# Kernel tuning notes

Hardware: AMD Instinct MI355X
Metric: run time of the kernel (lower is better)

## Reference

```python
import jax, jax.numpy as jnp
import numpy as np

BN_EPS = 1e-5

def _sign(x):
    # torch-style binarize with sign(0) -> +1 (deterministic)
    return jnp.where(x >= 0, 1.0, -1.0).astype(x.dtype)

def _binarize(x):
    # straight-through estimator: forward = sign(x), backward = identity
    return x + jax.lax.stop_gradient(_sign(x) - x)

def setup_inputs() -> dict:
    key = jax.random.key(0)
    k1, k2, k3, k4 = jax.random.split(key, 4)
    B, Cin, H, Wd = 64, 512, 32, 32  # Cin = in_planes*2
    Cout = 256                        # planes == in_planes
    x = jax.random.normal(k1, (B, Cin, H, Wd), jnp.float32)
    W = jax.random.normal(k2, (Cout, Cin, 3, 3), jnp.float32) * 0.05
    gamma = 1.0 + 0.1 * jax.random.normal(k3, (Cout,), jnp.float32)
    beta = 0.1 * jax.random.normal(k4, (Cout,), jnp.float32)
    return {"x": x, "W": W, "gamma": gamma, "beta": beta}

def reference(x, W, gamma, beta):
    inplanes = x.shape[1] // 2
    residual = x[:, :inplanes]  # first half of channels, pre-binarization
    xb = _binarize(x)
    wb = _binarize(W)
    out = jax.lax.conv_general_dilated(
        xb, wb, window_strides=(1, 1), padding=((1, 1), (1, 1)),
        dimension_numbers=("NCHW", "OIHW", "NCHW"))
    # BatchNorm2d in training mode (batch statistics over N,H,W per channel)
    mean = out.mean(axis=(0, 2, 3), keepdims=True)
    var = out.var(axis=(0, 2, 3), keepdims=True)
    out = (out - mean) * jax.lax.rsqrt(var + BN_EPS)
    out = out * gamma[None, :, None, None] + beta[None, :, None, None]
    out = out + residual
    return jnp.clip(out, -1.0, 1.0)  # Hardtanh
```

## Files before the change

kernel.cpp:

```cpp
#include <hip/hip_runtime.h>

#define CIN   512
#define COUT  256
#define HWDIM 32
#define NBATCH 64
#define PIX_PER_IMG (HWDIM * HWDIM)
#define NPIX (NBATCH * PIX_PER_IMG)

typedef __attribute__((ext_vector_type(4))) int   i32x4;
typedef __attribute__((ext_vector_type(8))) int   i32x8;
typedef __attribute__((ext_vector_type(4))) float f32x4;

#define OFF_XB4   ((size_t)0)
#define OFF_WB4   ((size_t)16777216)
#define OFF_CONV  ((size_t)17367040)
#define OFF_STATS ((size_t)50921472)
#define OFF_SCALE (OFF_STATS + 24576)
#define OFF_SHIFT (OFF_SCALE + 1024)
#define OFF_ZERO  (OFF_SHIFT + 1024)

#define NIB(v) ((v) >= 0.f ? 0x2u : 0xAu)

__global__ __launch_bounds__(256) void pack_x4_kernel(const float* __restrict__ x,
                                                      unsigned char* __restrict__ xb4) {
  const int plane = blockIdx.x;
  const int n = plane >> 5, h = plane & 31;
  __shared__ unsigned int tile[HWDIM * 66];
  const int t = threadIdx.x;
  const float* xp = x + (size_t)n * CIN * PIX_PER_IMG + (size_t)h * HWDIM;
#pragma unroll
  for (int it = 0; it < 2; ++it) {
    int idx = it * 256 + t;
    int cib = idx >> 3;
    int w4 = (idx & 7) << 2;
    unsigned n0 = 0, n1 = 0, n2 = 0, n3 = 0;
#pragma unroll
    for (int d = 0; d < 8; ++d) {
      float4 f = *reinterpret_cast<const float4*>(
          xp + (size_t)(cib * 8 + d) * PIX_PER_IMG + w4);
      n0 |= NIB(f.x) << (4 * d);
      n1 |= NIB(f.y) << (4 * d);
      n2 |= NIB(f.z) << (4 * d);
      n3 |= NIB(f.w) << (4 * d);
    }
    tile[(w4 + 0) * 66 + cib] = n0;
    tile[(w4 + 1) * 66 + cib] = n1;
    tile[(w4 + 2) * 66 + cib] = n2;
    tile[(w4 + 3) * 66 + cib] = n3;
  }
  __syncthreads();
  uint4* xo = reinterpret_cast<uint4*>(xb4 + (size_t)plane * (HWDIM * CIN / 2));
#pragma unroll
  for (int it = 0; it < 2; ++it) {
    int cc = it * 256 + t;
    int w = cc >> 4, c4 = (cc & 15) << 2;
    uint4 v = make_uint4(tile[w * 66 + c4], tile[w * 66 + c4 + 1],
                         tile[w * 66 + c4 + 2], tile[w * 66 + c4 + 3]);
    xo[cc] = v;
  }
}

__global__ __launch_bounds__(256) void pack_w4_kernel(const float* __restrict__ W,
                                                      unsigned int* __restrict__ wb4) {
  int idxu = blockIdx.x * 256 + threadIdx.x;
  int tap = idxu / (COUT * 64);
  int rem = idxu - tap * (COUT * 64);
  int co = rem >> 6;
  int ci0 = (rem & 63) << 3;
  unsigned nib = 0;
#pragma unroll
  for (int d = 0; d < 8; ++d) {
    float v = W[((size_t)co * CIN + ci0 + d) * 9 + tap];
    nib |= NIB(v) << (4 * d);
  }
  wb4[idxu] = nib;
}

#define BM 256
#define BKB 64
#define ABYTES (BM * BKB)
#define BUFB   (ABYTES + COUT * BKB)
#define LDS_TOTAL (4 * BUFB)
#define TAPB4 (COUT * (CIN / 2))

__device__ __forceinline__ void load16(const void* g, void* l) {
  __builtin_amdgcn_global_load_lds((const __attribute__((address_space(1))) void*)g,
                                   (__attribute__((address_space(3))) void*)l, 16, 0, 0);
}

__device__ __forceinline__ i32x8 up8(i32x4 v) {
  i32x8 r;
  r[0] = v[0]; r[1] = v[1]; r[2] = v[2]; r[3] = v[3];
  r[4] = 0;    r[5] = 0;    r[6] = 0;    r[7] = 0;
  return r;
}

__global__ __launch_bounds__(512, 2) void conv_kernel(
    const unsigned char* __restrict__ xb4,
    const unsigned char* __restrict__ wb4,
    short* __restrict__ cv,
    const unsigned char* __restrict__ zp,
    int* __restrict__ sum,
    unsigned long long* __restrict__ sumsq) {
  extern __shared__ signed char lds[];
  const int t = threadIdx.x;
  const int wid = t >> 6, lane = t & 63;
  const int b = blockIdx.x;
  const int nimg = b >> 2;
  const int h0 = (b & 3) * 8;

  const int wr = wid >> 2;
  const int wc = wid & 3;

  f32x4 acc[8][4];
#pragma unroll
  for (int m = 0; m < 8; ++m)
#pragma unroll
    for (int n = 0; n < 4; ++n) { f32x4 z = {0.f, 0.f, 0.f, 0.f}; acc[m][n] = z; }

  auto abase = [&](int tap, int c) -> const unsigned char* {
    int r = c >> 2;
    int sw = ((c & 3) ^ ((c >> 3) & 3)) << 4;
    int dh = tap / 3 - 1, dw = tap % 3 - 1;
    int hs = h0 + (r >> 5) + dh;
    int ws2 = (r & 31) + dw;
    bool ok = ((unsigned)hs < 32u) && ((unsigned)ws2 < 32u);
    return ok ? xb4 + (size_t)((nimg * 32 + hs) * 32 + ws2) * 256 + sw
              : zp + sw;
  };
  auto bbase = [&](int tap, int c) -> const unsigned char* {
    int co = c >> 2;
    int sw = ((c & 3) ^ ((c >> 3) & 3)) << 4;
    return wb4 + (size_t)tap * TAPB4 + (size_t)co * 256 + sw;
  };

  const int c0 = t, c1 = 512 + t;
  const unsigned char *a0 = abase(0, c0), *a1 = abase(0, c1);
  const unsigned char *b0 = bbase(0, c0), *b1 = bbase(0, c1);

  const int koff = (lane >> 4) << 4;
  const int ksw  = (((lane >> 1) & 3) << 4);
  int aoff[8], boff[4];
#pragma unroll
  for (int m = 0; m < 8; ++m) {
    int row = wr * 128 + m * 16 + (lane & 15);
    aoff[m] = row * BKB + (koff ^ ksw);
  }
#pragma unroll
  for (int n = 0; n < 4; ++n) {
    int col = wc * 64 + n * 16 + (lane & 15);
    boff[n] = ABYTES + col * BKB + (koff ^ ksw);
  }

  auto stage = [&](int buf, const unsigned char* A0, const unsigned char* A1,
                   const unsigned char* B0, const unsigned char* B1, int off) {
    signed char* dst = lds + buf * BUFB;
    load16(A0 + off, (void*)(dst + c0 * 16));
    load16(A1 + off, (void*)(dst + c1 * 16));
    load16(B0 + off, (void*)(dst + ABYTES + c0 * 16));
    load16(B1 + off, (void*)(dst + ABYTES + c1 * 16));
  };

  stage(0, a0, a1, b0, b1, 0);
  stage(1, a0, a1, b0, b1, 64);
  stage(2, a0, a1, b0, b1, 128);
  asm volatile("s_waitcnt vmcnt(8)" ::: "memory");
  __builtin_amdgcn_s_barrier();

  for (int tap = 0; tap < 9; ++tap) {
    const unsigned char *na0, *na1, *nb0, *nb1;
    if (tap < 8) {
      na0 = abase(tap + 1, c0); na1 = abase(tap + 1, c1);
      nb0 = b0 + TAPB4;         nb1 = b1 + TAPB4;
    } else {
      na0 = na1 = nb0 = nb1 = zp;
    }
#pragma unroll
    for (int j = 0; j < 4; ++j) {
      const int s = tap * 4 + j;
      if (j == 0)           stage((s + 3) & 3, a0, a1, b0, b1, 192);
      else if (tap < 8)     stage((s + 3) & 3, na0, na1, nb0, nb1, (j - 1) * 64);
      const signed char* base = lds + (s & 3) * BUFB;
      i32x4 af[8], bf[4];
#pragma unroll
      for (int n = 0; n < 4; ++n)
        bf[n] = *reinterpret_cast<const i32x4*>(base + boff[n]);
#pragma unroll
      for (int m = 0; m < 8; ++m)
        af[m] = *reinterpret_cast<const i32x4*>(base + aoff[m]);
      __builtin_amdgcn_s_setprio(1);
#pragma unroll
      for (int m = 0; m < 8; ++m)
#pragma unroll
        for (int n = 0; n < 4; ++n)
          acc[m][n] = __builtin_amdgcn_mfma_scale_f32_16x16x128_f8f6f4(
              up8(af[m]), up8(bf[n]), acc[m][n],
              4, 4,
              0, 0x7F7F7F7Fu,
              0, 0x7F7F7F7Fu);
      __builtin_amdgcn_s_setprio(0);
      if (tap < 8 || j == 0) asm volatile("s_waitcnt vmcnt(8)" ::: "memory");
      else if (j == 1)       asm volatile("s_waitcnt vmcnt(4)" ::: "memory");
      else                   asm volatile("s_waitcnt vmcnt(0)" ::: "memory");
      __builtin_amdgcn_s_barrier();
    }
    a0 = na0; a1 = na1; b0 = nb0; b1 = nb1;
  }

  const int P0 = b * BM;
#pragma unroll
  for (int m = 0; m < 8; ++m) {
#pragma unroll
    for (int n = 0; n < 4; ++n) {
      int row = wr * 128 + m * 16 + ((lane >> 4) << 2);
      int co = wc * 64 + n * 16 + (lane & 15);
      int P = P0 + row;
      int ni = P >> 10;
      int hw = P & 1023;
      short4 v = make_short4((short)(int)acc[m][n][0], (short)(int)acc[m][n][1],
                             (short)(int)acc[m][n][2], (short)(int)acc[m][n][3]);
      *reinterpret_cast<short4*>(cv + (((size_t)ni * COUT + co) << 10) + hw) = v;
    }
  }

  int* sumS = sum + (b & 7) * COUT;
  unsigned long long* sqS = sumsq + (b & 7) * COUT;
#pragma unroll
  for (int n = 0; n < 4; ++n) {
    int s1 = 0;
    long long s2 = 0;
#pragma unroll
    for (int m = 0; m < 8; ++m)
#pragma unroll
      for (int j = 0; j < 4; ++j) {
        int v = (int)acc[m][n][j];
        s1 += v;
        s2 += (long long)v * v;
      }
    s1 += __shfl_xor(s1, 16, 64);
    s1 += __shfl_xor(s1, 32, 64);
    s2 += __shfl_xor(s2, 16, 64);
    s2 += __shfl_xor(s2, 32, 64);
    if (lane < 16) {
      int c = wc * 64 + n * 16 + lane;
      atomicAdd(&sumS[c], s1);
      atomicAdd(&sqS[c], (unsigned long long)s2);
    }
  }
}

__global__ void stats_kernel(const int* __restrict__ sum,
                             const unsigned long long* __restrict__ sumsq,
                             const float* __restrict__ gamma,
                             const float* __restrict__ beta,
                             float* __restrict__ scale,
                             float* __restrict__ shift) {
  int co = threadIdx.x;
  long long s1 = 0, s2 = 0;
#pragma unroll
  for (int k = 0; k < 8; ++k) {
    s1 += sum[k * COUT + co];
    s2 += (long long)sumsq[k * COUT + co];
  }
  double cnt = (double)NPIX;
  double mean = (double)s1 / cnt;
  double ex2 = (double)s2 / cnt;
  double var = ex2 - mean * mean;
  double rs = 1.0 / sqrt(var + 1e-5);
  float g = gamma[co];
  scale[co] = (float)rs * g;
  shift[co] = beta[co] - (float)(mean * rs) * g;
}

__global__ __launch_bounds__(256) void final_kernel(const short* __restrict__ cv,
                                                    const float* __restrict__ x,
                                                    const float* __restrict__ scale,
                                                    const float* __restrict__ shift,
                                                    float* __restrict__ out) {
  size_t i = ((size_t)blockIdx.x * 256 + threadIdx.x) * 8;
  int co = (int)((i >> 10) & 255);
  size_t n = i >> 18;
  size_t hw = i & 1023;
  short4 c0 = *reinterpret_cast<const short4*>(cv + i);
  short4 c1 = *reinterpret_cast<const short4*>(cv + i + 4);
  const float* xr = x + ((n * CIN + co) << 10) + hw;
  float4 r0 = *reinterpret_cast<const float4*>(xr);
  float4 r1 = *reinterpret_cast<const float4*>(xr + 4);
  float sc = scale[co], sh = shift[co];
  float4 o0, o1;
  o0.x = fminf(1.f, fmaxf(-1.f, (float)c0.x * sc + sh + r0.x));
  o0.y = fminf(1.f, fmaxf(-1.f, (float)c0.y * sc + sh + r0.y));
  o0.z = fminf(1.f, fmaxf(-1.f, (float)c0.z * sc + sh + r0.z));
  o0.w = fminf(1.f, fmaxf(-1.f, (float)c0.w * sc + sh + r0.w));
  o1.x = fminf(1.f, fmaxf(-1.f, (float)c1.x * sc + sh + r1.x));
  o1.y = fminf(1.f, fmaxf(-1.f, (float)c1.y * sc + sh + r1.y));
  o1.z = fminf(1.f, fmaxf(-1.f, (float)c1.z * sc + sh + r1.z));
  o1.w = fminf(1.f, fmaxf(-1.f, (float)c1.w * sc + sh + r1.w));
  *reinterpret_cast<float4*>(out + i) = o0;
  *reinterpret_cast<float4*>(out + i + 4) = o1;
}

extern "C" void kernel_launch(void* const* d_in, const int* in_sizes, int n_in,
                              void* d_out, int out_size, void* d_ws, size_t ws_size,
                              hipStream_t stream) {
  const float* x     = (const float*)d_in[0];
  const float* W     = (const float*)d_in[1];
  const float* gamma = (const float*)d_in[2];
  const float* beta  = (const float*)d_in[3];
  float* out = (float*)d_out;
  char* ws = (char*)d_ws;

  unsigned char* xb4 = (unsigned char*)(ws + OFF_XB4);
  unsigned char* wb4 = (unsigned char*)(ws + OFF_WB4);
  short* cv = (short*)(ws + OFF_CONV);
  int* sum = (int*)(ws + OFF_STATS);
  unsigned long long* sumsq = (unsigned long long*)(ws + OFF_STATS + 8192);
  float* scale = (float*)(ws + OFF_SCALE);
  float* shift = (float*)(ws + OFF_SHIFT);
  unsigned char* zp = (unsigned char*)(ws + OFF_ZERO);

  hipFuncSetAttribute((const void*)conv_kernel,
                      hipFuncAttributeMaxDynamicSharedMemorySize, LDS_TOTAL);

  hipMemsetAsync(ws + OFF_STATS, 0, 27648, stream);

  pack_x4_kernel<<<NBATCH * HWDIM, 256, 0, stream>>>(x, xb4);
  pack_w4_kernel<<<(9 * COUT * 64) / 256, 256, 0, stream>>>(W, (unsigned int*)wb4);
  conv_kernel<<<NPIX / BM, 512, LDS_TOTAL, stream>>>(xb4, wb4, cv, zp, sum, sumsq);
  stats_kernel<<<1, 256, 0, stream>>>(sum, sumsq, gamma, beta, scale, shift);
  final_kernel<<<(NBATCH * COUT * PIX_PER_IMG) / (256 * 8), 256, 0, stream>>>(
      cv, x, scale, shift, out);
}
```

Before: 103.7 us.

## Restructure conv pipeline into half-tap double buffering and replace stat atomics

The conv main loop moves from a rolling 4-stage pipeline with a barrier after every k-slice to a scheme that loads two slices at a time and computes two, with full vmcnt(0) waits and two barriers per tap. The global atomics for BN sum and sum-of-squares become per-block partial writes that a single-block stats kernel reduces over 512 partials. This also removes the memset, and the zero page is now cleared inside an extra block of the weight pack kernel. The new pipeline exposes more load latency because of the full drains, and the serial 512-iteration reduction in one block adds latency to the stats step.

```diff
diff --git a/kernel.cpp b/kernel.cpp
--- a/kernel.cpp
+++ b/kernel.cpp
@@ -14,8 +14,9 @@
 #define OFF_XB4   ((size_t)0)
 #define OFF_WB4   ((size_t)16777216)
 #define OFF_CONV  ((size_t)17367040)
-#define OFF_STATS ((size_t)50921472)
-#define OFF_SCALE (OFF_STATS + 24576)
+#define OFF_PSUM  ((size_t)50921472)
+#define OFF_PSQ   ((size_t)51445760)
+#define OFF_SCALE ((size_t)52494336)
 #define OFF_SHIFT (OFF_SCALE + 1024)
 #define OFF_ZERO  (OFF_SHIFT + 1024)
 
@@ -61,7 +62,12 @@
 }
 
 __global__ __launch_bounds__(256) void pack_w4_kernel(const float* __restrict__ W,
-                                                      unsigned int* __restrict__ wb4) {
+                                                      unsigned int* __restrict__ wb4,
+                                                      unsigned int* __restrict__ zpw) {
+  if (blockIdx.x == 576) {
+    zpw[threadIdx.x] = 0u;
+    return;
+  }
   int idxu = blockIdx.x * 256 + threadIdx.x;
   int tap = idxu / (COUT * 64);
   int rem = idxu - tap * (COUT * 64);
@@ -100,8 +106,8 @@
     const unsigned char* __restrict__ wb4,
     short* __restrict__ cv,
     const unsigned char* __restrict__ zp,
-    int* __restrict__ sum,
-    unsigned long long* __restrict__ sumsq) {
+    int* __restrict__ psum,
+    long long* __restrict__ psq) {
   extern __shared__ signed char lds[];
   const int t = threadIdx.x;
   const int wid = t >> 6, lane = t & 63;
@@ -161,10 +167,31 @@
     load16(B1 + off, (void*)(dst + ABYTES + c1 * 16));
   };
 
+  auto compute = [&](int buf) {
+    const signed char* base = lds + buf * BUFB;
+    i32x4 af[8], bf[4];
+#pragma unroll
+    for (int n = 0; n < 4; ++n)
+      bf[n] = *reinterpret_cast<const i32x4*>(base + boff[n]);
+#pragma unroll
+    for (int m = 0; m < 8; ++m)
+      af[m] = *reinterpret_cast<const i32x4*>(base + aoff[m]);
+    __builtin_amdgcn_s_setprio(1);
+#pragma unroll
+    for (int m = 0; m < 8; ++m)
+#pragma unroll
+      for (int n = 0; n < 4; ++n)
+        acc[m][n] = __builtin_amdgcn_mfma_scale_f32_16x16x128_f8f6f4(
+            up8(af[m]), up8(bf[n]), acc[m][n],
+            4, 4,
+            0, 0x7F7F7F7Fu,
+            0, 0x7F7F7F7Fu);
+    __builtin_amdgcn_s_setprio(0);
+  };
+
   stage(0, a0, a1, b0, b1, 0);
   stage(1, a0, a1, b0, b1, 64);
-  stage(2, a0, a1, b0, b1, 128);
-  asm volatile("s_waitcnt vmcnt(8)" ::: "memory");
+  asm volatile("s_waitcnt vmcnt(0)" ::: "memory");
   __builtin_amdgcn_s_barrier();
 
   for (int tap = 0; tap < 9; ++tap) {
@@ -175,35 +202,21 @@
     } else {
       na0 = na1 = nb0 = nb1 = zp;
     }
-#pragma unroll
-    for (int j = 0; j < 4; ++j) {
-      const int s = tap * 4 + j;
-      if (j == 0)           stage((s + 3) & 3, a0, a1, b0, b1, 192);
-      else if (tap < 8)     stage((s + 3) & 3, na0, na1, nb0, nb1, (j - 1) * 64);
-      const signed char* base = lds + (s & 3) * BUFB;
-      i32x4 af[8], bf[4];
-#pragma unroll
-      for (int n = 0; n < 4; ++n)
-        bf[n] = *reinterpret_cast<const i32x4*>(base + boff[n]);
-#pragma unroll
-      for (int m = 0; m < 8; ++m)
-        af[m] = *reinterpret_cast<const i32x4*>(base + aoff[m]);
-      __builtin_amdgcn_s_setprio(1);
-#pragma unroll
-      for (int m = 0; m < 8; ++m)
-#pragma unroll
-        for (int n = 0; n < 4; ++n)
-          acc[m][n] = __builtin_amdgcn_mfma_scale_f32_16x16x128_f8f6f4(
-              up8(af[m]), up8(bf[n]), acc[m][n],
-              4, 4,
-              0, 0x7F7F7F7Fu,
-              0, 0x7F7F7F7Fu);
-      __builtin_amdgcn_s_setprio(0);
-      if (tap < 8 || j == 0) asm volatile("s_waitcnt vmcnt(8)" ::: "memory");
-      else if (j == 1)       asm volatile("s_waitcnt vmcnt(4)" ::: "memory");
-      else                   asm volatile("s_waitcnt vmcnt(0)" ::: "memory");
-      __builtin_amdgcn_s_barrier();
-    }
+    stage(2, a0, a1, b0, b1, 128);
+    stage(3, a0, a1, b0, b1, 192);
+    compute(0);
+    compute(1);
+    asm volatile("s_waitcnt vmcnt(0)" ::: "memory");
+    __builtin_amdgcn_s_barrier();
+    if (tap < 8) {
+      stage(0, na0, na1, nb0, nb1, 0);
+      stage(1, na0, na1, nb0, nb1, 64);
+    }
+    compute(2);
+    compute(3);
+    asm volatile("s_waitcnt vmcnt(0)" ::: "memory");
+    __builtin_amdgcn_s_barrier();
+
     a0 = na0; a1 = na1; b0 = nb0; b1 = nb1;
   }
 
@@ -223,8 +236,8 @@
     }
   }
 
-  int* sumS = sum + (b & 7) * COUT;
-  unsigned long long* sqS = sumsq + (b & 7) * COUT;
+  int* psumB = psum + (b * 2 + wr) * COUT;
+  long long* psqB = psq + (b * 2 + wr) * COUT;
 #pragma unroll
   for (int n = 0; n < 4; ++n) {
     int s1 = 0;
@@ -243,24 +256,23 @@
     s2 += __shfl_xor(s2, 32, 64);
     if (lane < 16) {
       int c = wc * 64 + n * 16 + lane;
-      atomicAdd(&sumS[c], s1);
-      atomicAdd(&sqS[c], (unsigned long long)s2);
-    }
-  }
-}
-
-__global__ void stats_kernel(const int* __restrict__ sum,
-                             const unsigned long long* __restrict__ sumsq,
+      psumB[c] = s1;
+      psqB[c] = s2;
+    }
+  }
+}
+
+__global__ void stats_kernel(const int* __restrict__ psum,
+                             const long long* __restrict__ psq,
                              const float* __restrict__ gamma,
                              const float* __restrict__ beta,
                              float* __restrict__ scale,
                              float* __restrict__ shift) {
   int co = threadIdx.x;
   long long s1 = 0, s2 = 0;
-#pragma unroll
-  for (int k = 0; k < 8; ++k) {
-    s1 += sum[k * COUT + co];
-    s2 += (long long)sumsq[k * COUT + co];
+  for (int k = 0; k < 512; ++k) {
+    s1 += psum[k * COUT + co];
+    s2 += psq[k * COUT + co];
   }
   double cnt = (double)NPIX;
   double mean = (double)s1 / cnt;
@@ -313,8 +325,8 @@
   unsigned char* xb4 = (unsigned char*)(ws + OFF_XB4);
   unsigned char* wb4 = (unsigned char*)(ws + OFF_WB4);
   short* cv = (short*)(ws + OFF_CONV);
-  int* sum = (int*)(ws + OFF_STATS);
-  unsigned long long* sumsq = (unsigned long long*)(ws + OFF_STATS + 8192);
+  int* psum = (int*)(ws + OFF_PSUM);
+  long long* psq = (long long*)(ws + OFF_PSQ);
   float* scale = (float*)(ws + OFF_SCALE);
   float* shift = (float*)(ws + OFF_SHIFT);
   unsigned char* zp = (unsigned char*)(ws + OFF_ZERO);
@@ -322,12 +334,10 @@
   hipFuncSetAttribute((const void*)conv_kernel,
                       hipFuncAttributeMaxDynamicSharedMemorySize, LDS_TOTAL);
 
-  hipMemsetAsync(ws + OFF_STATS, 0, 27648, stream);
-
   pack_x4_kernel<<<NBATCH * HWDIM, 256, 0, stream>>>(x, xb4);
-  pack_w4_kernel<<<(9 * COUT * 64) / 256, 256, 0, stream>>>(W, (unsigned int*)wb4);
-  conv_kernel<<<NPIX / BM, 512, LDS_TOTAL, stream>>>(xb4, wb4, cv, zp, sum, sumsq);
-  stats_kernel<<<1, 256, 0, stream>>>(sum, sumsq, gamma, beta, scale, shift);
+  pack_w4_kernel<<<577, 256, 0, stream>>>(W, (unsigned int*)wb4, (unsigned int*)zp);
+  conv_kernel<<<NPIX / BM, 512, LDS_TOTAL, stream>>>(xb4, wb4, cv, zp, psum, psq);
+  stats_kernel<<<1, 256, 0, stream>>>(psum, psq, gamma, beta, scale, shift);
   final_kernel<<<(NBATCH * COUT * PIX_PER_IMG) / (256 * 8), 256, 0, stream>>>(
       cv, x, scale, shift, out);
 }
```

Measured after the change: 129.2 us. +24.5%, slower.
